# Kernel tuning notes

Hardware: AMD Instinct MI355X
Metric: run time of the kernel (lower is better)

The kernel has to match this reference:

```python
import jax, jax.numpy as jnp
import numpy as np

B, S, D, H = 16, 1024, 512, 8
DEPTH = D // H  # 64


def setup_inputs() -> dict:
    key = jax.random.key(0)
    ks = jax.random.split(key, 12)
    std = 1.0 / np.sqrt(D)
    inp = {
        "q": jax.random.normal(ks[0], (B, S, D), dtype=jnp.float32),
        "k": jax.random.normal(ks[1], (B, S, D), dtype=jnp.float32),
        "v": jax.random.normal(ks[2], (B, S, D), dtype=jnp.float32),
        "mask": jax.random.randint(ks[3], (B, 1, 1, S), 0, 2, dtype=jnp.int32),
        "wq_w": jax.random.uniform(ks[4], (D, D), jnp.float32, -std, std),
        "wq_b": jax.random.uniform(ks[5], (D,), jnp.float32, -std, std),
        "wk_w": jax.random.uniform(ks[6], (D, D), jnp.float32, -std, std),
        "wk_b": jax.random.uniform(ks[7], (D,), jnp.float32, -std, std),
        "wv_w": jax.random.uniform(ks[8], (D, D), jnp.float32, -std, std),
        "wv_b": jax.random.uniform(ks[9], (D,), jnp.float32, -std, std),
        "wo_w": jax.random.uniform(ks[10], (D, D), jnp.float32, -std, std),
        "wo_b": jax.random.uniform(ks[11], (D,), jnp.float32, -std, std),
    }
    return inp


def reference(q, k, v, mask, wq_w, wq_b, wk_w, wk_b, wv_w, wv_b, wo_w, wo_b):
    b = q.shape[0]
    # QKV projections (torch Linear: x @ W.T + b), then split heads -> [B,H,S,depth]
    def proj(x, w, bias):
        y = x @ w.T + bias
        return y.reshape(b, -1, H, DEPTH).transpose(0, 2, 1, 3)

    qh, kh, vh = proj(q, wq_w, wq_b), proj(k, wk_w, wk_b), proj(v, wv_w, wv_b)

    # scaled dot-product attention with full [B,H,S,S] scores
    logits = jnp.einsum("bhqd,bhkd->bhqk", qh, kh) / jnp.sqrt(jnp.float32(DEPTH))
    logits = logits + mask.astype(logits.dtype) * -1e9
    # NOTE: original code softmaxes over dim=1 (the head axis) -- reproduced faithfully
    attn = jax.nn.softmax(logits, axis=1)
    ctx = jnp.einsum("bhqk,bhkd->bhqd", attn, vh)

    # merge heads and output projection
    ctx = ctx.transpose(0, 2, 1, 3).reshape(b, -1, D)
    out = ctx @ wo_w.T + wo_b
    return out, attn
```

## Files before the change

kernel.cpp:

```cpp
#include <hip/hip_runtime.h>
#include <hip/hip_bf16.h>
#include <math.h>

typedef __attribute__((ext_vector_type(8))) short short8;
typedef __attribute__((ext_vector_type(4))) float f32x4;
typedef __attribute__((ext_vector_type(4))) unsigned short ushort4_t;

#define MFMA16(a, b, c) __builtin_amdgcn_mfma_f32_16x16x32_bf16((a), (b), (c), 0, 0, 0)

#define GLOAD_LDS16(src, ldsbase)                                                     \
  __builtin_amdgcn_global_load_lds(                                                   \
      (const __attribute__((address_space(1))) void*)(src),                           \
      (__attribute__((address_space(3))) void*)(ldsbase), 16, 0, 0)

static __device__ __forceinline__ unsigned short f2bf(float f) {
  __hip_bfloat16 h = __float2bfloat16(f);
  unsigned short u;
  __builtin_memcpy(&u, &h, 2);
  return u;
}

static __device__ __forceinline__ float bf2f(unsigned short b) {
  union { unsigned u; float f; } v; v.u = ((unsigned)b) << 16;
  return v.f;
}

static __device__ __forceinline__ short8 cvt2v(f32x4 a, f32x4 b) {
  short8 t;
#pragma unroll
  for (int j = 0; j < 4; ++j) t[j] = (short)f2bf(a[j]);
#pragma unroll
  for (int j = 0; j < 4; ++j) t[4 + j] = (short)f2bf(b[j]);
  return t;
}

static __device__ __forceinline__ void lds_barrier() {
  __builtin_amdgcn_sched_barrier(0);
  asm volatile("s_waitcnt lgkmcnt(0)" ::: "memory");
  __builtin_amdgcn_s_barrier();
  __builtin_amdgcn_sched_barrier(0);
}

__global__ __launch_bounds__(256) void proj_gemm(
    const float* __restrict__ q, const float* __restrict__ k, const float* __restrict__ v,
    const float* __restrict__ wq, const float* __restrict__ wk, const float* __restrict__ wv,
    const float* __restrict__ bq, const float* __restrict__ bk, const float* __restrict__ bv,
    unsigned short* __restrict__ qh, unsigned short* __restrict__ kh,
    unsigned short* __restrict__ vt) {
  __shared__ unsigned short As[128 * 64], Ws[128 * 64];
  const int z = blockIdx.z;
  const float* A = z == 0 ? q : z == 1 ? k : v;
  const float* W = z == 0 ? wq : z == 1 ? wk : wv;
  const float* bias = z == 0 ? bq : z == 1 ? bk : bv;
  unsigned short* outp = z == 0 ? qh : z == 1 ? kh : vt;

  const int tid = threadIdx.x;
  const int wv_ = tid >> 6, lane = tid & 63;
  const int lr = lane & 15, lg = lane >> 4;
  const int m0 = blockIdx.x * 128, n0 = blockIdx.y * 128;
  const int wm = (wv_ >> 1) * 64, wn = (wv_ & 1) * 64;

  f32x4 acc[4][4] = {};

  for (int k0 = 0; k0 < 512; k0 += 64) {
    const int row = (tid >> 3), col = (tid & 7) * 8;
#pragma unroll
    for (int p = 0; p < 4; ++p) {
      const float* src = A + (size_t)(m0 + p * 32 + row) * 512 + k0 + col;
      f32x4 a0 = *(const f32x4*)src;
      f32x4 a1 = *(const f32x4*)(src + 4);
      *(short8*)&As[(p * 32 + row) * 64 + col] = cvt2v(a0, a1);
    }
#pragma unroll
    for (int p = 0; p < 4; ++p) {
      const float* src = W + (size_t)(n0 + p * 32 + row) * 512 + k0 + col;
      f32x4 a0 = *(const f32x4*)src;
      f32x4 a1 = *(const f32x4*)(src + 4);
      *(short8*)&Ws[(p * 32 + row) * 64 + col] = cvt2v(a0, a1);
    }
    __syncthreads();

#pragma unroll
    for (int ks = 0; ks < 2; ++ks) {
      short8 af[4], bw[4];
#pragma unroll
      for (int mi = 0; mi < 4; ++mi)
        af[mi] = *(const short8*)&As[(wm + mi * 16 + lr) * 64 + ks * 32 + lg * 8];
#pragma unroll
      for (int ni = 0; ni < 4; ++ni)
        bw[ni] = *(const short8*)&Ws[(wn + ni * 16 + lr) * 64 + ks * 32 + lg * 8];
#pragma unroll
      for (int mi = 0; mi < 4; ++mi)
#pragma unroll
        for (int ni = 0; ni < 4; ++ni)
          acc[mi][ni] = MFMA16(af[mi], bw[ni], acc[mi][ni]);
    }
    __syncthreads();
  }

#pragma unroll
  for (int ni = 0; ni < 4; ++ni) {
    const int c = n0 + wn + ni * 16 + lr;
    const float bv_ = bias[c];
#pragma unroll
    for (int mi = 0; mi < 4; ++mi) {
#pragma unroll
      for (int r = 0; r < 4; ++r) {
        const int rg = m0 + wm + mi * 16 + 4 * lg + r;
        const float val = acc[mi][ni][r] + bv_;
        const int bI = rg >> 10, s = rg & 1023, hI = c >> 6, d = c & 63;
        size_t addr;
        if (z < 2)
          addr = ((size_t)(bI * 8 + hI) << 16) + (s >> 4) * 1024 + (d >> 5) * 512 +
                 ((d >> 3) & 3) * 128 + (s & 15) * 8 + (d & 7);
        else
          addr = ((size_t)(bI * 8 + hI) << 16) + (s >> 6) * 4096 + (d >> 4) * 1024 +
                 ((s >> 5) & 1) * 512 + ((s >> 3) & 3) * 128 + (d & 15) * 8 + (s & 7);
        outp[addr] = f2bf(val);
      }
    }
  }
}

__global__ __launch_bounds__(256) void out_gemm(const unsigned short* __restrict__ A,
                                                const float* __restrict__ W,
                                                const float* __restrict__ bias,
                                                float* __restrict__ out_) {
  __shared__ unsigned short As[128 * 64], Ws[128 * 64];
  const int tid = threadIdx.x;
  const int wv_ = tid >> 6, lane = tid & 63;
  const int lr = lane & 15, lg = lane >> 4;
  const int m0 = blockIdx.x * 128, n0 = blockIdx.y * 128;
  const int wm = (wv_ >> 1) * 64, wn = (wv_ & 1) * 64;

  f32x4 acc[4][4] = {};

  for (int k0 = 0; k0 < 512; k0 += 64) {
#pragma unroll
    for (int p = 0; p < 4; ++p) {
      const int row = (p * 4 + wv_) * 8 + (lane >> 3);
      const int col = (lane & 7) * 8;
      GLOAD_LDS16(A + (size_t)(m0 + row) * 512 + k0 + col, &As[(p * 4 + wv_) * 512]);
    }
    const int row = (tid >> 3), col = (tid & 7) * 8;
#pragma unroll
    for (int p = 0; p < 4; ++p) {
      const float* src = W + (size_t)(n0 + p * 32 + row) * 512 + k0 + col;
      f32x4 a0 = *(const f32x4*)src;
      f32x4 a1 = *(const f32x4*)(src + 4);
      *(short8*)&Ws[(p * 32 + row) * 64 + col] = cvt2v(a0, a1);
    }
    __syncthreads();

#pragma unroll
    for (int ks = 0; ks < 2; ++ks) {
      short8 af[4], bw[4];
#pragma unroll
      for (int mi = 0; mi < 4; ++mi)
        af[mi] = *(const short8*)&As[(wm + mi * 16 + lr) * 64 + ks * 32 + lg * 8];
#pragma unroll
      for (int ni = 0; ni < 4; ++ni)
        bw[ni] = *(const short8*)&Ws[(wn + ni * 16 + lr) * 64 + ks * 32 + lg * 8];
#pragma unroll
      for (int mi = 0; mi < 4; ++mi)
#pragma unroll
        for (int ni = 0; ni < 4; ++ni)
          acc[mi][ni] = MFMA16(af[mi], bw[ni], acc[mi][ni]);
    }
    __syncthreads();
  }

#pragma unroll
  for (int ni = 0; ni < 4; ++ni) {
    const int c = n0 + wn + ni * 16 + lr;
    const float bv_ = bias[c];
#pragma unroll
    for (int mi = 0; mi < 4; ++mi)
#pragma unroll
      for (int r = 0; r < 4; ++r) {
        const int rg = m0 + wm + mi * 16 + 4 * lg + r;
        out_[(size_t)rg * 512 + c] = acc[mi][ni][r] + bv_;
      }
  }
}

__global__ __launch_bounds__(512, 4) void attn_fused(
    const unsigned short* __restrict__ qh, const unsigned short* __restrict__ kh,
    const unsigned short* __restrict__ vt, const int* __restrict__ mask,
    float* __restrict__ attn_out, unsigned short* __restrict__ ctx) {
  __shared__ unsigned short sb[2][8][32][72];
  __shared__ float mf[1024];

  const int tid = threadIdx.x;
  const int h = tid >> 6, lane = tid & 63;
  const int lr = lane & 15, lg = lane >> 4;

  const int lin = blockIdx.x + 32 * blockIdx.y;
  const int xcd = lin & 7, slot = lin >> 3;
  const int b = xcd + 8 * (slot >> 5);
  const int q0 = (slot & 31) * 32;

  const unsigned short* qb = qh + ((size_t)(b * 8 + h) << 16);
  const unsigned short* kb = kh + ((size_t)(b * 8 + h) << 16);
  const unsigned short* vb = vt + ((size_t)(b * 8 + h) << 16);

#pragma unroll
  for (int i = 0; i < 2; ++i)
    mf[tid + i * 512] = -1e9f * (float)mask[b * 1024 + tid + i * 512];

  short8 qf[2][2];
#pragma unroll
  for (int qi = 0; qi < 2; ++qi)
#pragma unroll
    for (int ks = 0; ks < 2; ++ks)
      qf[qi][ks] = *(const short8*)(qb + ((q0 >> 4) + qi) * 1024 + ks * 512 + lane * 8);

  const int sq = tid >> 4, sk4 = tid & 15;

  f32x4 apv[2][4] = {};

  lds_barrier();

  for (int kt = 0; kt < 16; ++kt) {
    const int k0 = kt * 64;
    unsigned short(*sc)[32][72] = sb[kt & 1];

    short8 kf[4][2];
#pragma unroll
    for (int ki = 0; ki < 4; ++ki)
#pragma unroll
      for (int ks = 0; ks < 2; ++ks)
        kf[ki][ks] = *(const short8*)(kb + ((k0 >> 4) + ki) * 1024 + ks * 512 + lane * 8);
    f32x4 aqk[4][2] = {};
#pragma unroll
    for (int ks = 0; ks < 2; ++ks)
#pragma unroll
      for (int ki = 0; ki < 4; ++ki)
#pragma unroll
        for (int qi = 0; qi < 2; ++qi)
          aqk[ki][qi] = MFMA16(kf[ki][ks], qf[qi][ks], aqk[ki][qi]);

#pragma unroll
    for (int ki = 0; ki < 4; ++ki) {
      f32x4 mv = *(const f32x4*)&mf[k0 + ki * 16 + 4 * lg];
#pragma unroll
      for (int qi = 0; qi < 2; ++qi) {
        ushort4_t pk;
#pragma unroll
        for (int r = 0; r < 4; ++r) pk[r] = f2bf(aqk[ki][qi][r] * 0.125f + mv[r]);
        *(ushort4_t*)&sc[h][qi * 16 + lr][ki * 16 + 4 * lg] = pk;
      }
    }

    short8 vf0[4];
#pragma unroll
    for (int ni = 0; ni < 4; ++ni)
      vf0[ni] = *(const short8*)(vb + kt * 4096 + ni * 1024 + lane * 8);

    lds_barrier();

    f32x4 e[8];
#pragma unroll
    for (int hh = 0; hh < 8; ++hh) {
      ushort4_t raw = *(const ushort4_t*)&sc[hh][sq][4 * sk4];
#pragma unroll
      for (int r = 0; r < 4; ++r) e[hh][r] = bf2f(raw[r]);
    }
    f32x4 mx = e[0];
#pragma unroll
    for (int hh = 1; hh < 8; ++hh)
#pragma unroll
      for (int r = 0; r < 4; ++r) mx[r] = fmaxf(mx[r], e[hh][r]);
    f32x4 s = {0.f, 0.f, 0.f, 0.f};
#pragma unroll
    for (int hh = 0; hh < 8; ++hh) {
#pragma unroll
      for (int r = 0; r < 4; ++r) e[hh][r] = __expf(e[hh][r] - mx[r]);
      s += e[hh];
    }
    f32x4 inv;
#pragma unroll
    for (int r = 0; r < 4; ++r) inv[r] = __builtin_amdgcn_rcpf(s[r]);

    float* abase = attn_out + (((size_t)(b * 8) * 1024 + q0 + sq) * 1024) + k0 + 4 * sk4;
#pragma unroll
    for (int hh = 0; hh < 8; ++hh) {
      f32x4 p = e[hh] * inv;
      __builtin_nontemporal_store(p, (f32x4*)(abase + ((size_t)hh << 20)));
      ushort4_t pk;
#pragma unroll
      for (int r = 0; r < 4; ++r) pk[r] = f2bf(p[r]);
      *(ushort4_t*)&sc[hh][sq][4 * sk4] = pk;
    }

    short8 vf1[4];
#pragma unroll
    for (int ni = 0; ni < 4; ++ni)
      vf1[ni] = *(const short8*)(vb + kt * 4096 + ni * 1024 + 512 + lane * 8);

    lds_barrier();

    short8 pf[2][2];
#pragma unroll
    for (int mi = 0; mi < 2; ++mi)
#pragma unroll
      for (int ks = 0; ks < 2; ++ks)
        pf[mi][ks] = *(const short8*)&sc[h][mi * 16 + lr][ks * 32 + 8 * lg];
#pragma unroll
    for (int mi = 0; mi < 2; ++mi)
#pragma unroll
      for (int ni = 0; ni < 4; ++ni)
        apv[mi][ni] = MFMA16(pf[mi][0], vf0[ni], apv[mi][ni]);
#pragma unroll
    for (int mi = 0; mi < 2; ++mi)
#pragma unroll
      for (int ni = 0; ni < 4; ++ni)
        apv[mi][ni] = MFMA16(pf[mi][1], vf1[ni], apv[mi][ni]);
  }

#pragma unroll
  for (int mi = 0; mi < 2; ++mi)
#pragma unroll
    for (int ni = 0; ni < 4; ++ni)
#pragma unroll
      for (int r = 0; r < 4; ++r) {
        const int row = q0 + mi * 16 + 4 * lg + r;
        const int col = h * 64 + ni * 16 + lr;
        ctx[((size_t)b * 1024 + row) * 512 + col] = f2bf(apv[mi][ni][r]);
      }
}

extern "C" void kernel_launch(void* const* d_in, const int* in_sizes, int n_in,
                              void* d_out, int out_size, void* d_ws, size_t ws_size,
                              hipStream_t stream) {
  const float* q = (const float*)d_in[0];
  const float* k = (const float*)d_in[1];
  const float* v = (const float*)d_in[2];
  const int* mask = (const int*)d_in[3];
  const float* wq_w = (const float*)d_in[4];
  const float* wq_b = (const float*)d_in[5];
  const float* wk_w = (const float*)d_in[6];
  const float* wk_b = (const float*)d_in[7];
  const float* wv_w = (const float*)d_in[8];
  const float* wv_b = (const float*)d_in[9];
  const float* wo_w = (const float*)d_in[10];
  const float* wo_b = (const float*)d_in[11];

  float* out = (float*)d_out;
  float* attn = out + (size_t)16 * 1024 * 512;

  unsigned short* qh = (unsigned short*)d_ws;
  unsigned short* kh = qh + (size_t)16 * 8 * 1024 * 64;
  unsigned short* vt = kh + (size_t)16 * 8 * 1024 * 64;
  unsigned short* ctx = vt + (size_t)16 * 8 * 1024 * 64;

  proj_gemm<<<dim3(128, 4, 3), dim3(256), 0, stream>>>(
      q, k, v, wq_w, wk_w, wv_w, wq_b, wk_b, wv_b, qh, kh, vt);
  attn_fused<<<dim3(32, 16), dim3(512), 0, stream>>>(qh, kh, vt, mask, attn, ctx);
  out_gemm<<<dim3(128, 4), dim3(256), 0, stream>>>(ctx, wo_w, wo_b, out);
}
```

Before: 234.7 us.

## Pre-convert weights to bf16 and vectorize GEMM epilogue stores

Adds a small kernel that converts the four fp32 weight matrices to bf16 once, so the projection and output GEMMs load weights directly into LDS with global_load_lds and skip per-tile conversion. It splits the QKV projection into separate Q/K and V kernels and swaps MFMA operand order so each lane holds four consecutive columns, which allows packed 8-byte bf16 and 16-byte fp32 stores in the epilogues instead of scalar scattered stores. The bf16 Q/K/V weights are stashed in the tail of the attn output buffer, relying on attn_fused overwriting that region afterward. This adds one more kernel launch and an ordering dependency on that scratch space.

Result: faster. 225.3 us (-4.0%).

```diff
diff --git a/kernel.cpp b/kernel.cpp
--- a/kernel.cpp
+++ b/kernel.cpp
@@ -41,18 +41,36 @@
   __builtin_amdgcn_sched_barrier(0);
 }
 
-__global__ __launch_bounds__(256) void proj_gemm(
-    const float* __restrict__ q, const float* __restrict__ k, const float* __restrict__ v,
-    const float* __restrict__ wq, const float* __restrict__ wk, const float* __restrict__ wv,
-    const float* __restrict__ bq, const float* __restrict__ bk, const float* __restrict__ bv,
-    unsigned short* __restrict__ qh, unsigned short* __restrict__ kh,
-    unsigned short* __restrict__ vt) {
+__global__ __launch_bounds__(256) void cvt_w(
+    const float* __restrict__ wq, const float* __restrict__ wk,
+    const float* __restrict__ wv, const float* __restrict__ wo,
+    unsigned short* __restrict__ wq16, unsigned short* __restrict__ wk16,
+    unsigned short* __restrict__ wv16, unsigned short* __restrict__ wo16) {
+  const int blk = blockIdx.x;
+  const float* src;
+  unsigned short* dst;
+  size_t base;
+  if (blk < 128)      { src = wq; dst = wq16; base = (size_t)blk * 2048; }
+  else if (blk < 256) { src = wk; dst = wk16; base = (size_t)(blk - 128) * 2048; }
+  else if (blk < 384) { src = wv; dst = wv16; base = (size_t)(blk - 256) * 2048; }
+  else                { src = wo; dst = wo16; base = (size_t)(blk - 384) * 2048; }
+  const size_t i = base + (size_t)threadIdx.x * 8;
+  f32x4 a = *(const f32x4*)(src + i);
+  f32x4 b = *(const f32x4*)(src + i + 4);
+  *(short8*)(dst + i) = cvt2v(a, b);
+}
+
+__global__ __launch_bounds__(256) void proj_qk(
+    const float* __restrict__ q, const float* __restrict__ k,
+    const unsigned short* __restrict__ wq16, const unsigned short* __restrict__ wk16,
+    const float* __restrict__ bq, const float* __restrict__ bk,
+    unsigned short* __restrict__ qh, unsigned short* __restrict__ kh) {
   __shared__ unsigned short As[128 * 64], Ws[128 * 64];
   const int z = blockIdx.z;
-  const float* A = z == 0 ? q : z == 1 ? k : v;
-  const float* W = z == 0 ? wq : z == 1 ? wk : wv;
-  const float* bias = z == 0 ? bq : z == 1 ? bk : bv;
-  unsigned short* outp = z == 0 ? qh : z == 1 ? kh : vt;
+  const float* A = z == 0 ? q : k;
+  const unsigned short* W16 = z == 0 ? wq16 : wk16;
+  const float* bias = z == 0 ? bq : bk;
+  unsigned short* outp = z == 0 ? qh : kh;
 
   const int tid = threadIdx.x;
   const int wv_ = tid >> 6, lane = tid & 63;
@@ -63,6 +81,12 @@
   f32x4 acc[4][4] = {};
 
   for (int k0 = 0; k0 < 512; k0 += 64) {
+#pragma unroll
+    for (int p = 0; p < 4; ++p) {
+      const int row = (p * 4 + wv_) * 8 + (lane >> 3);
+      const int col = (lane & 7) * 8;
+      GLOAD_LDS16(W16 + (size_t)(n0 + row) * 512 + k0 + col, &Ws[(p * 4 + wv_) * 512]);
+    }
     const int row = (tid >> 3), col = (tid & 7) * 8;
 #pragma unroll
     for (int p = 0; p < 4; ++p) {
@@ -71,12 +95,71 @@
       f32x4 a1 = *(const f32x4*)(src + 4);
       *(short8*)&As[(p * 32 + row) * 64 + col] = cvt2v(a0, a1);
     }
+    __syncthreads();
+
+#pragma unroll
+    for (int ks = 0; ks < 2; ++ks) {
+      short8 af[4], bw[4];
+#pragma unroll
+      for (int mi = 0; mi < 4; ++mi)
+        af[mi] = *(const short8*)&As[(wm + mi * 16 + lr) * 64 + ks * 32 + lg * 8];
+#pragma unroll
+      for (int ni = 0; ni < 4; ++ni)
+        bw[ni] = *(const short8*)&Ws[(wn + ni * 16 + lr) * 64 + ks * 32 + lg * 8];
+#pragma unroll
+      for (int ni = 0; ni < 4; ++ni)
+#pragma unroll
+        for (int mi = 0; mi < 4; ++mi)
+          acc[ni][mi] = MFMA16(bw[ni], af[mi], acc[ni][mi]);
+    }
+    __syncthreads();
+  }
+
+  const int hI = (n0 + wn) >> 6;
+#pragma unroll
+  for (int ni = 0; ni < 4; ++ni) {
+    const int d0 = ni * 16 + 4 * lg;
+    f32x4 bvv = *(const f32x4*)&bias[n0 + wn + d0];
+#pragma unroll
+    for (int mi = 0; mi < 4; ++mi) {
+      const int s = m0 + wm + mi * 16 + lr;
+      const int bI = s >> 10, srow = s & 1023;
+      size_t addr = ((size_t)(bI * 8 + hI) << 16) + (srow >> 4) * 1024 +
+                    (d0 >> 5) * 512 + ((d0 >> 3) & 3) * 128 + lr * 8 + (d0 & 7);
+      ushort4_t pk;
+#pragma unroll
+      for (int r = 0; r < 4; ++r) pk[r] = f2bf(acc[ni][mi][r] + bvv[r]);
+      *(ushort4_t*)&outp[addr] = pk;
+    }
+  }
+}
+
+__global__ __launch_bounds__(256) void proj_v(
+    const float* __restrict__ v, const unsigned short* __restrict__ wv16,
+    const float* __restrict__ bv, unsigned short* __restrict__ vt) {
+  __shared__ unsigned short As[128 * 64], Ws[128 * 64];
+  const int tid = threadIdx.x;
+  const int wv_ = tid >> 6, lane = tid & 63;
+  const int lr = lane & 15, lg = lane >> 4;
+  const int m0 = blockIdx.x * 128, n0 = blockIdx.y * 128;
+  const int wm = (wv_ >> 1) * 64, wn = (wv_ & 1) * 64;
+
+  f32x4 acc[4][4] = {};
+
+  for (int k0 = 0; k0 < 512; k0 += 64) {
 #pragma unroll
     for (int p = 0; p < 4; ++p) {
-      const float* src = W + (size_t)(n0 + p * 32 + row) * 512 + k0 + col;
+      const int row = (p * 4 + wv_) * 8 + (lane >> 3);
+      const int col = (lane & 7) * 8;
+      GLOAD_LDS16(wv16 + (size_t)(n0 + row) * 512 + k0 + col, &Ws[(p * 4 + wv_) * 512]);
+    }
+    const int row = (tid >> 3), col = (tid & 7) * 8;
+#pragma unroll
+    for (int p = 0; p < 4; ++p) {
+      const float* src = v + (size_t)(m0 + p * 32 + row) * 512 + k0 + col;
       f32x4 a0 = *(const f32x4*)src;
       f32x4 a1 = *(const f32x4*)(src + 4);
-      *(short8*)&Ws[(p * 32 + row) * 64 + col] = cvt2v(a0, a1);
+      *(short8*)&As[(p * 32 + row) * 64 + col] = cvt2v(a0, a1);
     }
     __syncthreads();
 
@@ -98,32 +181,26 @@
     __syncthreads();
   }
 
+  const int hI = (n0 + wn) >> 6;
 #pragma unroll
   for (int ni = 0; ni < 4; ++ni) {
-    const int c = n0 + wn + ni * 16 + lr;
-    const float bv_ = bias[c];
+    const float bv_ = bv[n0 + wn + ni * 16 + lr];
 #pragma unroll
     for (int mi = 0; mi < 4; ++mi) {
-#pragma unroll
-      for (int r = 0; r < 4; ++r) {
-        const int rg = m0 + wm + mi * 16 + 4 * lg + r;
-        const float val = acc[mi][ni][r] + bv_;
-        const int bI = rg >> 10, s = rg & 1023, hI = c >> 6, d = c & 63;
-        size_t addr;
-        if (z < 2)
-          addr = ((size_t)(bI * 8 + hI) << 16) + (s >> 4) * 1024 + (d >> 5) * 512 +
-                 ((d >> 3) & 3) * 128 + (s & 15) * 8 + (d & 7);
-        else
-          addr = ((size_t)(bI * 8 + hI) << 16) + (s >> 6) * 4096 + (d >> 4) * 1024 +
-                 ((s >> 5) & 1) * 512 + ((s >> 3) & 3) * 128 + (d & 15) * 8 + (s & 7);
-        outp[addr] = f2bf(val);
-      }
+      const int s0 = m0 + wm + mi * 16 + 4 * lg;
+      const int bI = s0 >> 10, srow = s0 & 1023;
+      size_t addr = ((size_t)(bI * 8 + hI) << 16) + (srow >> 6) * 4096 + ni * 1024 +
+                    ((srow >> 5) & 1) * 512 + ((srow >> 3) & 3) * 128 + lr * 8 + (srow & 7);
+      ushort4_t pk;
+#pragma unroll
+      for (int r = 0; r < 4; ++r) pk[r] = f2bf(acc[mi][ni][r] + bv_);
+      *(ushort4_t*)&vt[addr] = pk;
     }
   }
 }
 
 __global__ __launch_bounds__(256) void out_gemm(const unsigned short* __restrict__ A,
-                                                const float* __restrict__ W,
+                                                const unsigned short* __restrict__ W16,
                                                 const float* __restrict__ bias,
                                                 float* __restrict__ out_) {
   __shared__ unsigned short As[128 * 64], Ws[128 * 64];
@@ -141,14 +218,7 @@
       const int row = (p * 4 + wv_) * 8 + (lane >> 3);
       const int col = (lane & 7) * 8;
       GLOAD_LDS16(A + (size_t)(m0 + row) * 512 + k0 + col, &As[(p * 4 + wv_) * 512]);
-    }
-    const int row = (tid >> 3), col = (tid & 7) * 8;
-#pragma unroll
-    for (int p = 0; p < 4; ++p) {
-      const float* src = W + (size_t)(n0 + p * 32 + row) * 512 + k0 + col;
-      f32x4 a0 = *(const f32x4*)src;
-      f32x4 a1 = *(const f32x4*)(src + 4);
-      *(short8*)&Ws[(p * 32 + row) * 64 + col] = cvt2v(a0, a1);
+      GLOAD_LDS16(W16 + (size_t)(n0 + row) * 512 + k0 + col, &Ws[(p * 4 + wv_) * 512]);
     }
     __syncthreads();
 
@@ -162,25 +232,24 @@
       for (int ni = 0; ni < 4; ++ni)
         bw[ni] = *(const short8*)&Ws[(wn + ni * 16 + lr) * 64 + ks * 32 + lg * 8];
 #pragma unroll
-      for (int mi = 0; mi < 4; ++mi)
-#pragma unroll
-        for (int ni = 0; ni < 4; ++ni)
-          acc[mi][ni] = MFMA16(af[mi], bw[ni], acc[mi][ni]);
+      for (int ni = 0; ni < 4; ++ni)
+#pragma unroll
+        for (int mi = 0; mi < 4; ++mi)
+          acc[ni][mi] = MFMA16(bw[ni], af[mi], acc[ni][mi]);
     }
     __syncthreads();
   }
 
 #pragma unroll
   for (int ni = 0; ni < 4; ++ni) {
-    const int c = n0 + wn + ni * 16 + lr;
-    const float bv_ = bias[c];
-#pragma unroll
-    for (int mi = 0; mi < 4; ++mi)
-#pragma unroll
-      for (int r = 0; r < 4; ++r) {
-        const int rg = m0 + wm + mi * 16 + 4 * lg + r;
-        out_[(size_t)rg * 512 + c] = acc[mi][ni][r] + bv_;
-      }
+    const int c0 = n0 + wn + ni * 16 + 4 * lg;
+    f32x4 bvv = *(const f32x4*)&bias[c0];
+#pragma unroll
+    for (int mi = 0; mi < 4; ++mi) {
+      const int rg = m0 + wm + mi * 16 + lr;
+      f32x4 val = acc[ni][mi] + bvv;
+      *(f32x4*)&out_[(size_t)rg * 512 + c0] = val;
+    }
   }
 }
 
@@ -349,13 +418,20 @@
   float* out = (float*)d_out;
   float* attn = out + (size_t)16 * 1024 * 512;
 
+  unsigned short* wq16 = (unsigned short*)(attn + (134217728 - 393216));
+  unsigned short* wk16 = wq16 + 262144;
+  unsigned short* wv16 = wk16 + 262144;
+
   unsigned short* qh = (unsigned short*)d_ws;
   unsigned short* kh = qh + (size_t)16 * 8 * 1024 * 64;
   unsigned short* vt = kh + (size_t)16 * 8 * 1024 * 64;
   unsigned short* ctx = vt + (size_t)16 * 8 * 1024 * 64;
-
-  proj_gemm<<<dim3(128, 4, 3), dim3(256), 0, stream>>>(
-      q, k, v, wq_w, wk_w, wv_w, wq_b, wk_b, wv_b, qh, kh, vt);
+  unsigned short* wo16 = ctx + (size_t)16 * 1024 * 512;
+
+  cvt_w<<<dim3(512), dim3(256), 0, stream>>>(wq_w, wk_w, wv_w, wo_w,
+                                             wq16, wk16, wv16, wo16);
+  proj_qk<<<dim3(128, 4, 2), dim3(256), 0, stream>>>(q, k, wq16, wk16, wq_b, wk_b, qh, kh);
+  proj_v<<<dim3(128, 4), dim3(256), 0, stream>>>(v, wv16, wv_b, vt);
   attn_fused<<<dim3(32, 16), dim3(512), 0, stream>>>(qh, kh, vt, mask, attn, ctx);
-  out_gemm<<<dim3(128, 4), dim3(256), 0, stream>>>(ctx, wo_w, wo_b, out);
-}
+  out_gemm<<<dim3(128, 4), dim3(256), 0, stream>>>(ctx, wo16, wo_b, out);
+}
```
